# Kernel tuning notes

Measured on AMD Instinct MI355X. Metric: run time of the kernel, lower is better.

Reference implementation:

```python
import jax, jax.numpy as jnp
import numpy as np

N_NODES = 100000


def gcn_layer(x, row, col, ew, W, b, n_nodes):
    # PyG GCNConv: add self-loops (weight 1), symmetric normalization
    # deg^{-1/2}[row] * w * deg^{-1/2}[col], linear transform, scatter-add to col.
    loop = jnp.arange(n_nodes, dtype=row.dtype)
    row_f = jnp.concatenate([row, loop])
    col_f = jnp.concatenate([col, loop])
    ew_f = jnp.concatenate([ew, jnp.ones((n_nodes,), dtype=ew.dtype)])
    deg = jax.ops.segment_sum(ew_f, col_f, num_segments=n_nodes)  # [N]
    dinv = jnp.where(deg > 0, jax.lax.rsqrt(deg), 0.0)
    norm = dinv[row_f] * ew_f * dinv[col_f]  # [E+N]
    h = x @ W  # [N, F_out]
    msg = norm[:, None] * h[row_f]  # [E+N, F_out]
    out = jax.ops.segment_sum(msg, col_f, num_segments=n_nodes)
    return out + b


def setup_inputs() -> dict:
    key = jax.random.key(0)
    ks = jax.random.split(key, 6)
    n, e, d_in, d_h = N_NODES, 3200000, 128, 16
    x = jax.random.normal(ks[0], (n, d_in), dtype=jnp.float32)
    edge_index = jax.random.randint(ks[1], (2, e), 0, n, dtype=jnp.int64)
    edge_weight = jax.random.uniform(ks[2], (e,), dtype=jnp.float32)
    W1 = jax.random.normal(ks[3], (d_in, d_h), dtype=jnp.float32) * (1.0 / np.sqrt(d_in))
    b1 = jnp.zeros((d_h,), dtype=jnp.float32)
    W2 = jax.random.normal(ks[4], (d_h, 1), dtype=jnp.float32) * (1.0 / np.sqrt(d_h))
    b2 = jnp.zeros((1,), dtype=jnp.float32)
    return {"x": x, "edge_index": edge_index, "edge_weight": edge_weight,
            "W1": W1, "b1": b1, "W2": W2, "b2": b2}


def reference(x, edge_index, edge_weight, W1, b1, W2, b2):
    row, col = edge_index[0], edge_index[1]
    n = x.shape[0]
    h = gcn_layer(x, row, col, edge_weight, W1, b1, n)
    h = jax.nn.relu(h)
    out = gcn_layer(h, row, col, edge_weight, W2, b2, n)
    return out.squeeze(-1)  # [N]
```

## Files before the change

### kernel.cpp

```cpp
#include <hip/hip_runtime.h>


#define DH 16
#define BSH 7
#define BNODES 128
#define NB_MAX 784
#define CHUNK 4096

__global__ __launch_bounds__(256) void k_Ahist(const int* __restrict__ col,
                                               int* __restrict__ gCnt, int E, int NB) {
    __shared__ int lh[NB_MAX];
    const int tid = threadIdx.x;
    for (int i = tid; i < NB; i += 256) lh[i] = 0;
    __syncthreads();
    const int base = blockIdx.x * CHUNK;
    #pragma unroll
    for (int k = 0; k < 16; ++k) {
        int e = base + tid + 256 * k;
        if (e < E) atomicAdd(&lh[col[e] >> BSH], 1);
    }
    __syncthreads();
    for (int i = tid; i < NB; i += 256) {
        int v = lh[i];
        if (v) atomicAdd(&gCnt[i], v);
    }
}

__global__ __launch_bounds__(1024) void k_Ascan(const int* __restrict__ gCnt,
                                                int* __restrict__ gBase,
                                                int* __restrict__ gCursor,
                                                int NB, int E) {
    __shared__ int s[1024];
    const int t = threadIdx.x;
    int v = (t < NB) ? gCnt[t] : 0;
    s[t] = v;
    __syncthreads();
    for (int off = 1; off < 1024; off <<= 1) {
        int u = (t >= off) ? s[t - off] : 0;
        __syncthreads();
        s[t] += u;
        __syncthreads();
    }
    if (t < NB) {
        int ex = s[t] - v;
        gBase[t] = ex;
        gCursor[t] = ex;
    }
    if (t == 0) gBase[NB] = E;
}

__global__ __launch_bounds__(256) void k_Ascatter(const int* __restrict__ row,
                                                  const int* __restrict__ col,
                                                  const float* __restrict__ ew,
                                                  int* __restrict__ gCursor,
                                                  uint2* __restrict__ edata,
                                                  int E, int NB) {
    __shared__ int lh[NB_MAX];
    __shared__ int lbase[NB_MAX];
    __shared__ int lcur[NB_MAX];
    __shared__ int tsum[256];
    __shared__ unsigned short sbuck[CHUNK];
    __shared__ uint2 stage[CHUNK];
    const int tid = threadIdx.x;
    for (int i = tid; i < NB; i += 256) lh[i] = 0;
    __syncthreads();
    const int base = blockIdx.x * CHUNK;
    int r_[16], c_[16];
    float w_[16];
    #pragma unroll
    for (int k = 0; k < 16; ++k) {
        int e = base + tid + 256 * k;
        bool ok = e < E;
        c_[k] = ok ? col[e] : -1;
        r_[k] = ok ? row[e] : 0;
        w_[k] = ok ? ew[e] : 0.f;
        if (ok) atomicAdd(&lh[c_[k] >> BSH], 1);
    }
    __syncthreads();
    const int t0 = tid * 4;
    int c0 = (t0 + 0 < NB) ? lh[t0 + 0] : 0;
    int c1 = (t0 + 1 < NB) ? lh[t0 + 1] : 0;
    int c2 = (t0 + 2 < NB) ? lh[t0 + 2] : 0;
    int c3 = (t0 + 3 < NB) ? lh[t0 + 3] : 0;
    int mysum = c0 + c1 + c2 + c3;
    tsum[tid] = mysum;
    __syncthreads();
    for (int off = 1; off < 256; off <<= 1) {
        int u = (tid >= off) ? tsum[tid - off] : 0;
        __syncthreads();
        tsum[tid] += u;
        __syncthreads();
    }
    int p = tsum[tid] - mysum;
    if (t0 + 0 < NB) { lbase[t0 + 0] = p; lcur[t0 + 0] = p; } p += c0;
    if (t0 + 1 < NB) { lbase[t0 + 1] = p; lcur[t0 + 1] = p; } p += c1;
    if (t0 + 2 < NB) { lbase[t0 + 2] = p; lcur[t0 + 2] = p; } p += c2;
    if (t0 + 3 < NB) { lbase[t0 + 3] = p; lcur[t0 + 3] = p; } p += c3;
    __syncthreads();
    for (int b = tid; b < NB; b += 256) {
        int cnt = lcur[b];
    }
    for (int b = tid; b < NB; b += 256) {
        int cnt = lh[b];
        if (cnt) {
            int g = atomicAdd(&gCursor[b], cnt);
            lh[b] = g - lbase[b];
        }
    }
    __syncthreads();
    #pragma unroll
    for (int k = 0; k < 16; ++k) {
        if (c_[k] >= 0) {
            int b = c_[k] >> BSH;
            unsigned rem = (unsigned)(c_[k] & (BNODES - 1));
            int sp = atomicAdd(&lcur[b], 1);
            stage[sp] = make_uint2((unsigned)r_[k] | (rem << 20), __float_as_uint(w_[k]));
            sbuck[sp] = (unsigned short)b;
        }
    }
    __syncthreads();
    int nE = E - base;
    if (nE > CHUNK) nE = CHUNK;
    for (int j = tid; j < nE; j += 256)
        edata[lh[sbuck[j]] + j] = stage[j];
}

__global__ __launch_bounds__(256) void k_deg(const int* __restrict__ gBase,
                                             const uint2* __restrict__ edata,
                                             float* __restrict__ dinv, int N) {
    __shared__ float dg[BNODES];
    const int tid = threadIdx.x;
    if (tid < BNODES) dg[tid] = 0.f;
    __syncthreads();
    const int s = gBase[blockIdx.x], e = gBase[blockIdx.x + 1];
    for (int i = s + tid; i < e; i += 256) {
        uint2 ed = edata[i];
        atomicAdd(&dg[ed.x >> 20], __uint_as_float(ed.y));
    }
    __syncthreads();
    int node = (blockIdx.x << BSH) + tid;
    if (tid < BNODES && node < N) dinv[node] = rsqrtf(dg[tid] + 1.0f);
}

__global__ __launch_bounds__(256) void k_h1(const float* __restrict__ x,
                                            const float* __restrict__ W1,
                                            const float* __restrict__ dinv,
                                            float* __restrict__ hd) {
    __shared__ float Ws[128 * DH];
    __shared__ float xs[16 * 132];
    const int t = threadIdx.x;
    const int node0 = blockIdx.x * 16;
    #pragma unroll
    for (int i = 0; i < 8; ++i) Ws[t + 256 * i] = W1[t + 256 * i];
    const float4* xg = (const float4*)(x + (size_t)node0 * 128);
    #pragma unroll
    for (int it = 0; it < 2; ++it) {
        int idx = t + 256 * it;
        int n = idx >> 5, k4 = idx & 31;
        float4 v = xg[n * 32 + k4];
        *(float4*)(&xs[n * 132 + k4 * 4]) = v;
    }
    __syncthreads();
    const int node = t >> 4, feat = t & 15;
    const float* xr = &xs[node * 132];
    float acc = 0.f;
    #pragma unroll 8
    for (int k = 0; k < 128; ++k) acc += xr[k] * Ws[k * DH + feat];
    const int v = node0 + node;
    hd[(size_t)v * DH + feat] = dinv[v] * acc;
}

__global__ __launch_bounds__(256) void k_gather1(
    const int* __restrict__ gBase, const uint2* __restrict__ edata,
    const float* __restrict__ hd, const float* __restrict__ dinv,
    const float* __restrict__ b1, const float* __restrict__ W2,
    float* __restrict__ q, int N) {
    __shared__ float acc[BNODES][DH + 1];
    __shared__ float b1s[DH], W2s[DH];
    const int tid = threadIdx.x;
    if (tid < DH) { b1s[tid] = b1[tid]; W2s[tid] = W2[tid]; }
    for (int i = tid; i < BNODES * (DH + 1); i += 256) ((float*)acc)[i] = 0.f;
    __syncthreads();
    const int b = blockIdx.x;
    const int s = gBase[b], e = gBase[b + 1];
    for (int i = s + tid; i < e; i += 512) {
        uint2 ed0 = edata[i];
        int i1 = i + 256;
        uint2 ed1 = (i1 < e) ? edata[i1] : make_uint2(0u, 0u);
        int r0 = ed0.x & 0xFFFFF, rem0 = ed0.x >> 20;
        int r1 = ed1.x & 0xFFFFF, rem1 = ed1.x >> 20;
        float w0 = __uint_as_float(ed0.y), w1 = __uint_as_float(ed1.y);
        const float4* h0 = (const float4*)(hd + (size_t)r0 * DH);
        const float4* h1 = (const float4*)(hd + (size_t)r1 * DH);
        float4 A0 = h0[0], B0 = h0[1], C0 = h0[2], D0 = h0[3];
        float4 A1 = h1[0], B1 = h1[1], C1 = h1[2], D1 = h1[3];
        float* a0 = acc[rem0];
        atomicAdd(a0 + 0,  w0 * A0.x); atomicAdd(a0 + 1,  w0 * A0.y);
        atomicAdd(a0 + 2,  w0 * A0.z); atomicAdd(a0 + 3,  w0 * A0.w);
        atomicAdd(a0 + 4,  w0 * B0.x); atomicAdd(a0 + 5,  w0 * B0.y);
        atomicAdd(a0 + 6,  w0 * B0.z); atomicAdd(a0 + 7,  w0 * B0.w);
        atomicAdd(a0 + 8,  w0 * C0.x); atomicAdd(a0 + 9,  w0 * C0.y);
        atomicAdd(a0 + 10, w0 * C0.z); atomicAdd(a0 + 11, w0 * C0.w);
        atomicAdd(a0 + 12, w0 * D0.x); atomicAdd(a0 + 13, w0 * D0.y);
        atomicAdd(a0 + 14, w0 * D0.z); atomicAdd(a0 + 15, w0 * D0.w);
        float* a1 = acc[rem1];
        atomicAdd(a1 + 0,  w1 * A1.x); atomicAdd(a1 + 1,  w1 * A1.y);
        atomicAdd(a1 + 2,  w1 * A1.z); atomicAdd(a1 + 3,  w1 * A1.w);
        atomicAdd(a1 + 4,  w1 * B1.x); atomicAdd(a1 + 5,  w1 * B1.y);
        atomicAdd(a1 + 6,  w1 * B1.z); atomicAdd(a1 + 7,  w1 * B1.w);
        atomicAdd(a1 + 8,  w1 * C1.x); atomicAdd(a1 + 9,  w1 * C1.y);
        atomicAdd(a1 + 10, w1 * C1.z); atomicAdd(a1 + 11, w1 * C1.w);
        atomicAdd(a1 + 12, w1 * D1.x); atomicAdd(a1 + 13, w1 * D1.y);
        atomicAdd(a1 + 14, w1 * D1.z); atomicAdd(a1 + 15, w1 * D1.w);
    }
    __syncthreads();
    int node = (b << BSH) + tid;
    if (tid < BNODES && node < N) {
        float dc = dinv[node];
        const float4* hs = (const float4*)(hd + (size_t)node * DH);
        float t = 0.f;
        #pragma unroll
        for (int qd = 0; qd < 4; ++qd) {
            float4 hv = hs[qd];
            int f = qd * 4;
            t += fmaxf(dc * (acc[tid][f + 0] + hv.x) + b1s[f + 0], 0.f) * W2s[f + 0];
            t += fmaxf(dc * (acc[tid][f + 1] + hv.y) + b1s[f + 1], 0.f) * W2s[f + 1];
            t += fmaxf(dc * (acc[tid][f + 2] + hv.z) + b1s[f + 2], 0.f) * W2s[f + 2];
            t += fmaxf(dc * (acc[tid][f + 3] + hv.w) + b1s[f + 3], 0.f) * W2s[f + 3];
        }
        q[node] = dc * t;
    }
}

__global__ __launch_bounds__(256) void k_gather2(
    const int* __restrict__ gBase, const uint2* __restrict__ edata,
    const float* __restrict__ dinv, const float* __restrict__ q,
    const float* __restrict__ b2, float* __restrict__ out, int N) {
    __shared__ float a2[BNODES];
    const int tid = threadIdx.x;
    if (tid < BNODES) a2[tid] = 0.f;
    __syncthreads();
    const int s = gBase[blockIdx.x], e = gBase[blockIdx.x + 1];
    for (int i = s + tid; i < e; i += 512) {
        uint2 ed0 = edata[i];
        int i1 = i + 256;
        uint2 ed1 = (i1 < e) ? edata[i1] : make_uint2(0u, 0u);
        float v0 = __uint_as_float(ed0.y) * q[ed0.x & 0xFFFFF];
        float v1 = __uint_as_float(ed1.y) * q[ed1.x & 0xFFFFF];
        atomicAdd(&a2[ed0.x >> 20], v0);
        atomicAdd(&a2[ed1.x >> 20], v1);
    }
    __syncthreads();
    int node = (blockIdx.x << BSH) + tid;
    if (tid < BNODES && node < N)
        out[node] = b2[0] + dinv[node] * (a2[tid] + q[node]);
}

extern "C" void kernel_launch(void* const* d_in, const int* in_sizes, int n_in,
                              void* d_out, int out_size, void* d_ws, size_t ws_size,
                              hipStream_t stream) {
    const float* x  = (const float*)d_in[0];
    const int*   ei = (const int*)d_in[1];
    const float* ew = (const float*)d_in[2];
    const float* W1 = (const float*)d_in[3];
    const float* b1 = (const float*)d_in[4];
    const float* W2 = (const float*)d_in[5];
    const float* b2 = (const float*)d_in[6];
    float* out = (float*)d_out;

    const int N = in_sizes[0] / 128;
    const int E = in_sizes[2];
    const int* row = ei;
    const int* col = ei + E;
    const int NB = (N + BNODES - 1) >> BSH;

    int* gCnt    = (int*)d_ws;
    int* gBase   = gCnt + NB;
    int* gCursor = gBase + NB + 1;
    float* dinv  = (float*)(gCursor + NB);
    float* hd    = dinv + N;
    float* q     = hd + (size_t)16 * N;
    uintptr_t ep = (uintptr_t)(q + N);
    ep = (ep + 7) & ~(uintptr_t)7;
    uint2* edata = (uint2*)ep;

    const int ablocks = (E + CHUNK - 1) / CHUNK;

    hipMemsetAsync(gCnt, 0, (size_t)NB * sizeof(int), stream);
    k_Ahist<<<ablocks, 256, 0, stream>>>(col, gCnt, E, NB);
    k_Ascan<<<1, 1024, 0, stream>>>(gCnt, gBase, gCursor, NB, E);
    k_Ascatter<<<ablocks, 256, 0, stream>>>(row, col, ew, gCursor, edata, E, NB);
    k_deg<<<NB, 256, 0, stream>>>(gBase, edata, dinv, N);
    k_h1<<<N / 16, 256, 0, stream>>>(x, W1, dinv, hd);
    k_gather1<<<NB, 256, 0, stream>>>(gBase, edata, hd, dinv, b1, W2, q, N);
    k_gather2<<<NB, 256, 0, stream>>>(gBase, edata, dinv, q, b2, out, N);
}
```

Before: 592.8 us.

## Halve node buckets, split gather work across slices with partial-sum reduction

Node buckets shrink from 128 to 64 nodes and each bucket's edge range is now split across several blocks (2 for degree and layer-2 gather, 4 for layer-1 gather). The blocks combine their results through global atomics or a partial buffer reduced in a new finalize kernel. The layer-1 gather now assigns one feature per lane, with 16 lanes per edge, instead of one edge per thread doing 16 LDS atomics. The aim is more parallelism and fewer LDS atomic conflicts. In exchange it adds an extra kernel, a partial buffer round-trip, global atomics, and moves rsqrt into the h1 kernel.

```diff
diff --git a/kernel.cpp b/kernel.cpp
--- a/kernel.cpp
+++ b/kernel.cpp
@@ -2,10 +2,12 @@
 
 
 #define DH 16
-#define BSH 7
-#define BNODES 128
-#define NB_MAX 784
+#define BSH 6
+#define BNODES 64
+#define NB_MAX 1568
 #define CHUNK 4096
+#define HCHUNK 8192
+#define NSLICE 4
 
 __global__ __launch_bounds__(256) void k_Ahist(const int* __restrict__ col,
                                                int* __restrict__ gCnt, int E, int NB) {
@@ -13,9 +15,9 @@
     const int tid = threadIdx.x;
     for (int i = tid; i < NB; i += 256) lh[i] = 0;
     __syncthreads();
-    const int base = blockIdx.x * CHUNK;
-    #pragma unroll
-    for (int k = 0; k < 16; ++k) {
+    const int base = blockIdx.x * HCHUNK;
+    #pragma unroll
+    for (int k = 0; k < 32; ++k) {
         int e = base + tid + 256 * k;
         if (e < E) atomicAdd(&lh[col[e] >> BSH], 1);
     }
@@ -32,7 +34,10 @@
                                                 int NB, int E) {
     __shared__ int s[1024];
     const int t = threadIdx.x;
-    int v = (t < NB) ? gCnt[t] : 0;
+    const int i0 = 2 * t, i1 = 2 * t + 1;
+    int a = (i0 < NB) ? gCnt[i0] : 0;
+    int b = (i1 < NB) ? gCnt[i1] : 0;
+    int v = a + b;
     s[t] = v;
     __syncthreads();
     for (int off = 1; off < 1024; off <<= 1) {
@@ -41,11 +46,9 @@
         s[t] += u;
         __syncthreads();
     }
-    if (t < NB) {
-        int ex = s[t] - v;
-        gBase[t] = ex;
-        gCursor[t] = ex;
-    }
+    int ex = s[t] - v;
+    if (i0 < NB) { gBase[i0] = ex;     gCursor[i0] = ex; }
+    if (i1 < NB) { gBase[i1] = ex + a; gCursor[i1] = ex + a; }
     if (t == 0) gBase[NB] = E;
 }
 
@@ -77,12 +80,14 @@
         if (ok) atomicAdd(&lh[c_[k] >> BSH], 1);
     }
     __syncthreads();
-    const int t0 = tid * 4;
-    int c0 = (t0 + 0 < NB) ? lh[t0 + 0] : 0;
-    int c1 = (t0 + 1 < NB) ? lh[t0 + 1] : 0;
-    int c2 = (t0 + 2 < NB) ? lh[t0 + 2] : 0;
-    int c3 = (t0 + 3 < NB) ? lh[t0 + 3] : 0;
-    int mysum = c0 + c1 + c2 + c3;
+    const int t0 = tid * 8;
+    int c8[8];
+    int mysum = 0;
+    #pragma unroll
+    for (int k = 0; k < 8; ++k) {
+        c8[k] = (t0 + k < NB) ? lh[t0 + k] : 0;
+        mysum += c8[k];
+    }
     tsum[tid] = mysum;
     __syncthreads();
     for (int off = 1; off < 256; off <<= 1) {
@@ -92,14 +97,12 @@
         __syncthreads();
     }
     int p = tsum[tid] - mysum;
-    if (t0 + 0 < NB) { lbase[t0 + 0] = p; lcur[t0 + 0] = p; } p += c0;
-    if (t0 + 1 < NB) { lbase[t0 + 1] = p; lcur[t0 + 1] = p; } p += c1;
-    if (t0 + 2 < NB) { lbase[t0 + 2] = p; lcur[t0 + 2] = p; } p += c2;
-    if (t0 + 3 < NB) { lbase[t0 + 3] = p; lcur[t0 + 3] = p; } p += c3;
-    __syncthreads();
-    for (int b = tid; b < NB; b += 256) {
-        int cnt = lcur[b];
-    }
+    #pragma unroll
+    for (int k = 0; k < 8; ++k) {
+        if (t0 + k < NB) { lbase[t0 + k] = p; lcur[t0 + k] = p; }
+        p += c8[k];
+    }
+    __syncthreads();
     for (int b = tid; b < NB; b += 256) {
         int cnt = lh[b];
         if (cnt) {
@@ -127,24 +130,27 @@
 
 __global__ __launch_bounds__(256) void k_deg(const int* __restrict__ gBase,
                                              const uint2* __restrict__ edata,
-                                             float* __restrict__ dinv, int N) {
+                                             float* __restrict__ deg, int N) {
     __shared__ float dg[BNODES];
     const int tid = threadIdx.x;
     if (tid < BNODES) dg[tid] = 0.f;
     __syncthreads();
-    const int s = gBase[blockIdx.x], e = gBase[blockIdx.x + 1];
-    for (int i = s + tid; i < e; i += 256) {
+    const int b = blockIdx.x;
+    const int s = gBase[b], e = gBase[b + 1];
+    for (int i = s + blockIdx.y * 256 + tid; i < e; i += 512) {
         uint2 ed = edata[i];
         atomicAdd(&dg[ed.x >> 20], __uint_as_float(ed.y));
     }
     __syncthreads();
-    int node = (blockIdx.x << BSH) + tid;
-    if (tid < BNODES && node < N) dinv[node] = rsqrtf(dg[tid] + 1.0f);
+    int node = (b << BSH) + tid;
+    if (tid < BNODES && node < N && dg[tid] != 0.f)
+        atomicAdd(&deg[node], dg[tid]);
 }
 
 __global__ __launch_bounds__(256) void k_h1(const float* __restrict__ x,
                                             const float* __restrict__ W1,
-                                            const float* __restrict__ dinv,
+                                            const float* __restrict__ deg,
+                                            float* __restrict__ dinv,
                                             float* __restrict__ hd) {
     __shared__ float Ws[128 * DH];
     __shared__ float xs[16 * 132];
@@ -167,51 +173,57 @@
     #pragma unroll 8
     for (int k = 0; k < 128; ++k) acc += xr[k] * Ws[k * DH + feat];
     const int v = node0 + node;
-    hd[(size_t)v * DH + feat] = dinv[v] * acc;
+    const float di = rsqrtf(deg[v] + 1.0f);
+    if (feat == 0) dinv[v] = di;
+    hd[(size_t)v * DH + feat] = di * acc;
 }
 
 __global__ __launch_bounds__(256) void k_gather1(
     const int* __restrict__ gBase, const uint2* __restrict__ edata,
-    const float* __restrict__ hd, const float* __restrict__ dinv,
-    const float* __restrict__ b1, const float* __restrict__ W2,
-    float* __restrict__ q, int N) {
+    const float* __restrict__ hd, float* __restrict__ partial) {
+    __shared__ float acc[BNODES][DH + 1];
+    const int tid = threadIdx.x;
+    for (int i = tid; i < BNODES * (DH + 1); i += 256) ((float*)acc)[i] = 0.f;
+    __syncthreads();
+    const int b = blockIdx.x, sl = blockIdx.y;
+    const int s = gBase[b], e = gBase[b + 1];
+    const int g = tid >> 4, f = tid & 15;
+    for (int i = s + sl * 16 + g; i < e; i += 256) {
+        uint2 e0 = edata[i];
+        uint2 e1 = (i + 64  < e) ? edata[i + 64]  : make_uint2(0u, 0u);
+        uint2 e2 = (i + 128 < e) ? edata[i + 128] : make_uint2(0u, 0u);
+        uint2 e3 = (i + 192 < e) ? edata[i + 192] : make_uint2(0u, 0u);
+        float v0 = __uint_as_float(e0.y) * hd[(size_t)(e0.x & 0xFFFFF) * DH + f];
+        float v1 = __uint_as_float(e1.y) * hd[(size_t)(e1.x & 0xFFFFF) * DH + f];
+        float v2 = __uint_as_float(e2.y) * hd[(size_t)(e2.x & 0xFFFFF) * DH + f];
+        float v3 = __uint_as_float(e3.y) * hd[(size_t)(e3.x & 0xFFFFF) * DH + f];
+        atomicAdd(&acc[e0.x >> 20][f], v0);
+        atomicAdd(&acc[e1.x >> 20][f], v1);
+        atomicAdd(&acc[e2.x >> 20][f], v2);
+        atomicAdd(&acc[e3.x >> 20][f], v3);
+    }
+    __syncthreads();
+    float* ps = partial + ((size_t)b * NSLICE + sl) * (DH * BNODES);
+    for (int i = tid; i < DH * BNODES; i += 256)
+        ps[i] = acc[i >> 4][i & 15];
+}
+
+__global__ __launch_bounds__(256) void k_fin1(
+    const float* __restrict__ partial, const float* __restrict__ dinv,
+    const float* __restrict__ hd, const float* __restrict__ b1,
+    const float* __restrict__ W2, const float* __restrict__ b2,
+    float* __restrict__ q, float* __restrict__ out, int N) {
     __shared__ float acc[BNODES][DH + 1];
     __shared__ float b1s[DH], W2s[DH];
     const int tid = threadIdx.x;
     if (tid < DH) { b1s[tid] = b1[tid]; W2s[tid] = W2[tid]; }
-    for (int i = tid; i < BNODES * (DH + 1); i += 256) ((float*)acc)[i] = 0.f;
-    __syncthreads();
     const int b = blockIdx.x;
-    const int s = gBase[b], e = gBase[b + 1];
-    for (int i = s + tid; i < e; i += 512) {
-        uint2 ed0 = edata[i];
-        int i1 = i + 256;
-        uint2 ed1 = (i1 < e) ? edata[i1] : make_uint2(0u, 0u);
-        int r0 = ed0.x & 0xFFFFF, rem0 = ed0.x >> 20;
-        int r1 = ed1.x & 0xFFFFF, rem1 = ed1.x >> 20;
-        float w0 = __uint_as_float(ed0.y), w1 = __uint_as_float(ed1.y);
-        const float4* h0 = (const float4*)(hd + (size_t)r0 * DH);
-        const float4* h1 = (const float4*)(hd + (size_t)r1 * DH);
-        float4 A0 = h0[0], B0 = h0[1], C0 = h0[2], D0 = h0[3];
-        float4 A1 = h1[0], B1 = h1[1], C1 = h1[2], D1 = h1[3];
-        float* a0 = acc[rem0];
-        atomicAdd(a0 + 0,  w0 * A0.x); atomicAdd(a0 + 1,  w0 * A0.y);
-        atomicAdd(a0 + 2,  w0 * A0.z); atomicAdd(a0 + 3,  w0 * A0.w);
-        atomicAdd(a0 + 4,  w0 * B0.x); atomicAdd(a0 + 5,  w0 * B0.y);
-        atomicAdd(a0 + 6,  w0 * B0.z); atomicAdd(a0 + 7,  w0 * B0.w);
-        atomicAdd(a0 + 8,  w0 * C0.x); atomicAdd(a0 + 9,  w0 * C0.y);
-        atomicAdd(a0 + 10, w0 * C0.z); atomicAdd(a0 + 11, w0 * C0.w);
-        atomicAdd(a0 + 12, w0 * D0.x); atomicAdd(a0 + 13, w0 * D0.y);
-        atomicAdd(a0 + 14, w0 * D0.z); atomicAdd(a0 + 15, w0 * D0.w);
-        float* a1 = acc[rem1];
-        atomicAdd(a1 + 0,  w1 * A1.x); atomicAdd(a1 + 1,  w1 * A1.y);
-        atomicAdd(a1 + 2,  w1 * A1.z); atomicAdd(a1 + 3,  w1 * A1.w);
-        atomicAdd(a1 + 4,  w1 * B1.x); atomicAdd(a1 + 5,  w1 * B1.y);
-        atomicAdd(a1 + 6,  w1 * B1.z); atomicAdd(a1 + 7,  w1 * B1.w);
-        atomicAdd(a1 + 8,  w1 * C1.x); atomicAdd(a1 + 9,  w1 * C1.y);
-        atomicAdd(a1 + 10, w1 * C1.z); atomicAdd(a1 + 11, w1 * C1.w);
-        atomicAdd(a1 + 12, w1 * D1.x); atomicAdd(a1 + 13, w1 * D1.y);
-        atomicAdd(a1 + 14, w1 * D1.z); atomicAdd(a1 + 15, w1 * D1.w);
+    const float* ps = partial + (size_t)b * NSLICE * (DH * BNODES);
+    for (int i = tid; i < DH * BNODES; i += 256) {
+        float s = 0.f;
+        #pragma unroll
+        for (int sl = 0; sl < NSLICE; ++sl) s += ps[sl * (DH * BNODES) + i];
+        acc[i >> 4][i & 15] = s;
     }
     __syncthreads();
     int node = (b << BSH) + tid;
@@ -228,32 +240,30 @@
             t += fmaxf(dc * (acc[tid][f + 2] + hv.z) + b1s[f + 2], 0.f) * W2s[f + 2];
             t += fmaxf(dc * (acc[tid][f + 3] + hv.w) + b1s[f + 3], 0.f) * W2s[f + 3];
         }
-        q[node] = dc * t;
+        float qq = dc * t;
+        q[node] = qq;
+        out[node] = b2[0] + dc * qq;
     }
 }
 
 __global__ __launch_bounds__(256) void k_gather2(
     const int* __restrict__ gBase, const uint2* __restrict__ edata,
     const float* __restrict__ dinv, const float* __restrict__ q,
-    const float* __restrict__ b2, float* __restrict__ out, int N) {
+    float* __restrict__ out, int N) {
     __shared__ float a2[BNODES];
     const int tid = threadIdx.x;
     if (tid < BNODES) a2[tid] = 0.f;
     __syncthreads();
-    const int s = gBase[blockIdx.x], e = gBase[blockIdx.x + 1];
-    for (int i = s + tid; i < e; i += 512) {
-        uint2 ed0 = edata[i];
-        int i1 = i + 256;
-        uint2 ed1 = (i1 < e) ? edata[i1] : make_uint2(0u, 0u);
-        float v0 = __uint_as_float(ed0.y) * q[ed0.x & 0xFFFFF];
-        float v1 = __uint_as_float(ed1.y) * q[ed1.x & 0xFFFFF];
-        atomicAdd(&a2[ed0.x >> 20], v0);
-        atomicAdd(&a2[ed1.x >> 20], v1);
-    }
-    __syncthreads();
-    int node = (blockIdx.x << BSH) + tid;
-    if (tid < BNODES && node < N)
-        out[node] = b2[0] + dinv[node] * (a2[tid] + q[node]);
+    const int b = blockIdx.x;
+    const int s = gBase[b], e = gBase[b + 1];
+    for (int i = s + blockIdx.y * 256 + tid; i < e; i += 512) {
+        uint2 ed = edata[i];
+        atomicAdd(&a2[ed.x >> 20], __uint_as_float(ed.y) * q[ed.x & 0xFFFFF]);
+    }
+    __syncthreads();
+    int node = (b << BSH) + tid;
+    if (tid < BNODES && node < N && a2[tid] != 0.f)
+        atomicAdd(&out[node], dinv[node] * a2[tid]);
 }
 
 extern "C" void kernel_launch(void* const* d_in, const int* in_sizes, int n_in,
@@ -273,25 +283,30 @@
     const int* row = ei;
     const int* col = ei + E;
     const int NB = (N + BNODES - 1) >> BSH;
+    const int NBp = (NB + 3) & ~3;
 
     int* gCnt    = (int*)d_ws;
-    int* gBase   = gCnt + NB;
-    int* gCursor = gBase + NB + 1;
-    float* dinv  = (float*)(gCursor + NB);
+    float* deg   = (float*)(gCnt + NBp);
+    int* gBase   = (int*)(deg + N);
+    int* gCursor = gBase + NBp;
+    float* dinv  = (float*)(gCursor + NBp);
     float* hd    = dinv + N;
     float* q     = hd + (size_t)16 * N;
-    uintptr_t ep = (uintptr_t)(q + N);
-    ep = (ep + 7) & ~(uintptr_t)7;
+    float* partial = q + N;
+    uintptr_t ep = (uintptr_t)(partial + (size_t)NB * NSLICE * (DH * BNODES));
+    ep = (ep + 15) & ~(uintptr_t)15;
     uint2* edata = (uint2*)ep;
 
-    const int ablocks = (E + CHUNK - 1) / CHUNK;
-
-    hipMemsetAsync(gCnt, 0, (size_t)NB * sizeof(int), stream);
-    k_Ahist<<<ablocks, 256, 0, stream>>>(col, gCnt, E, NB);
+    const int hblocks = (E + HCHUNK - 1) / HCHUNK;
+    const int sblocks = (E + CHUNK - 1) / CHUNK;
+
+    hipMemsetAsync(gCnt, 0, ((size_t)NBp + N) * sizeof(int), stream);
+    k_Ahist<<<hblocks, 256, 0, stream>>>(col, gCnt, E, NB);
     k_Ascan<<<1, 1024, 0, stream>>>(gCnt, gBase, gCursor, NB, E);
-    k_Ascatter<<<ablocks, 256, 0, stream>>>(row, col, ew, gCursor, edata, E, NB);
-    k_deg<<<NB, 256, 0, stream>>>(gBase, edata, dinv, N);
-    k_h1<<<N / 16, 256, 0, stream>>>(x, W1, dinv, hd);
-    k_gather1<<<NB, 256, 0, stream>>>(gBase, edata, hd, dinv, b1, W2, q, N);
-    k_gather2<<<NB, 256, 0, stream>>>(gBase, edata, dinv, q, b2, out, N);
-}
+    k_Ascatter<<<sblocks, 256, 0, stream>>>(row, col, ew, gCursor, edata, E, NB);
+    k_deg<<<dim3(NB, 2), 256, 0, stream>>>(gBase, edata, deg, N);
+    k_h1<<<N / 16, 256, 0, stream>>>(x, W1, deg, dinv, hd);
+    k_gather1<<<dim3(NB, NSLICE), 256, 0, stream>>>(gBase, edata, hd, partial);
+    k_fin1<<<NB, 256, 0, stream>>>(partial, dinv, hd, b1, W2, b2, q, out, N);
+    k_gather2<<<dim3(NB, 2), 256, 0, stream>>>(gBase, edata, dinv, q, out, N);
+}
```

Result: faster. 523.8 us (-11.6%).
